# Optimization experiments

Hardware: AMD Instinct MI355X
Metric: run time of the kernel (lower is better)

Reference implementation:

```python
import jax, jax.numpy as jnp
import numpy as np

NUM_CLUSTERS = 56
HEIGHT = 224
WIDTH = 224
BATCH = 32
FEAT_C = 64


def setup_inputs() -> dict:
    key = jax.random.key(0)
    combined_features = jax.random.normal(key, (BATCH, FEAT_C + 1, HEIGHT, WIDTH), dtype=jnp.float32)
    # std parameter init: num_clusters / sqrt(H*W)
    std = jnp.asarray(NUM_CLUSTERS / (HEIGHT * WIDTH) ** 0.5, dtype=jnp.float32)
    return {"combined_features": combined_features, "std": std}


def _sobel(edges):
    # edges: [B,1,H,W], 3x3 sobel with padding=1 (fixed, non-learnable filters)
    kx = jnp.array([[-1., 0., 1.], [-2., 0., 2.], [-1., 0., 1.]], jnp.float32)[None, None]
    ky = jnp.array([[-1., -2., -1.], [0., 0., 0.], [1., 2., 1.]], jnp.float32)[None, None]
    conv = lambda k: jax.lax.conv_general_dilated(edges, k, (1, 1), [(1, 1), (1, 1)])
    return conv(kx), conv(ky)


def reference(combined_features, std):
    B, Cp1, H, W = combined_features.shape
    K = NUM_CLUSTERS
    edges = combined_features[:, -1:]      # [B,1,H,W]
    features = combined_features[:, :-1]   # [B,C,H,W]

    # --- centroid seeding from edge map ---
    Gx, Gy = _sobel(edges)
    grad_mag = jnp.sqrt(Gx ** 2 + Gy ** 2)
    inverted = 1.0 - 0.5 * grad_mag                      # [B,1,H,W]
    # adaptive_avg_pool2d to (K,K); H,W divisible by K -> exact reshape-mean
    pooled = inverted[:, 0].reshape(B, K, H // K, K, W // K).mean(axis=(2, 4))  # [B,K,K]
    flat = pooled.reshape(B, K * K)
    _, idx = jax.lax.top_k(flat, K)                      # [B,K]
    sy = (idx // K).astype(jnp.float32) / K              # [B,K] in [0,1)
    sx = (idx % K).astype(jnp.float32) / K

    # --- spatial gaussian distance: separable over y and x ---
    y = (jnp.arange(H, dtype=jnp.float32) / H)[None, None, :, None]  # [1,1,H,1]
    x = (jnp.arange(W, dtype=jnp.float32) / W)[None, None, None, :]  # [1,1,1,W]
    dy = y - sy[:, :, None, None]                        # [B,K,H,1]
    dx = x - sx[:, :, None, None]                        # [B,K,1,W]
    # gauss2d(a,b,std) = (exp(-(a/std)^2) + exp(-(b/std)^2)) / 2
    spatial = (jnp.exp(-(dy / std) ** 2) + jnp.exp(-(dx / std) ** 2)) * 0.5  # [B,K,H,W]

    # --- feature distance of each pixel to global mean feature (eps=1e-6 as in F.pairwise_distance) ---
    centroid = features.mean(axis=(2, 3))                # [B,C]
    fdist = jnp.sqrt(jnp.sum((features - centroid[:, :, None, None] + 1e-6) ** 2, axis=1))  # [B,H,W]

    combined = spatial + fdist[:, None]                  # [B,K,H,W]
    markers = jax.nn.softmax(combined, axis=1)           # softmax over clusters
    return markers
```

## Files before the change

kernel.cpp:

```cpp
#include <hip/hip_runtime.h>
#include <math.h>

#define NCLUS 56
#define HH 224
#define WW 224
#define BB 32
#define CELLS (NCLUS * NCLUS)
#define HW (HH * WW)

typedef float f32x4 __attribute__((ext_vector_type(4)));

__global__ __launch_bounds__(256) void pool_kernel(const float* __restrict__ cf,
                                                   float* __restrict__ pooled) {
    __shared__ float lds[18][226];
    int b = blockIdx.x / 14;
    int grp = blockIdx.x - b * 14;
    int tid = threadIdx.x;
    const float* e = cf + ((size_t)b * 65 + 64) * HW;

    int y0 = grp * 16 - 1;
    for (int t = tid; t < 18 * 224; t += 256) {
        int r = t / 224;
        int c = t - r * 224;
        int y = y0 + r;
        lds[r][c + 1] = (y >= 0 && y < HH) ? e[y * WW + c] : 0.0f;
    }
    if (tid < 18) { lds[tid][0] = 0.0f; lds[tid][225] = 0.0f; }
    __syncthreads();

    if (tid >= 224) return;
    int lby = tid / 56;
    int bx = tid - lby * 56;
    int r0 = lby * 4;
    int c0 = bx * 4;

    float patch[6][6];
#pragma unroll
    for (int i = 0; i < 6; ++i)
#pragma unroll
        for (int j = 0; j < 6; ++j) patch[i][j] = lds[r0 + i][c0 + j];

    float s = 0.0f;
#pragma unroll
    for (int iy = 0; iy < 4; ++iy) {
#pragma unroll
        for (int ix = 0; ix < 4; ++ix) {
            float gx = (patch[iy][ix + 2] - patch[iy][ix])
                     + 2.0f * (patch[iy + 1][ix + 2] - patch[iy + 1][ix])
                     + (patch[iy + 2][ix + 2] - patch[iy + 2][ix]);
            float gy = (patch[iy + 2][ix] - patch[iy][ix])
                     + 2.0f * (patch[iy + 2][ix + 1] - patch[iy][ix + 1])
                     + (patch[iy + 2][ix + 2] - patch[iy][ix + 2]);
            float gm = sqrtf(gx * gx + gy * gy);
            s += 1.0f - 0.5f * gm;
        }
    }
    pooled[b * CELLS + (grp * 4 + lby) * NCLUS + bx] = s * 0.0625f;
}

__global__ __launch_bounds__(256) void topk_tables_kernel(
        const float* __restrict__ pooled, const float* __restrict__ stdp,
        float* __restrict__ Fx, float* __restrict__ Fy) {
    int b = blockIdx.x;
    int tid = threadIdx.x;
    __shared__ unsigned long long list[CELLS];
    __shared__ float sy_s[NCLUS], sx_s[NCLUS];
    __shared__ unsigned nlist_s;
    if (tid == 0) nlist_s = 0;

    if (tid < 64) {
        unsigned hi[49];
#pragma unroll
        for (int j = 0; j < 49; ++j) {
            int i = j * 64 + tid;
            unsigned u = __float_as_uint(pooled[b * CELLS + i]);
            hi[j] = (u & 0x80000000u) ? ~u : (u | 0x80000000u);
        }
        unsigned prefix = 0;
        unsigned cnt = CELLS;
        for (int bit = 31; bit >= 0; --bit) {
            if (cnt <= 448u) break;
            unsigned cand = prefix | (1u << bit);
            unsigned c = 0;
#pragma unroll
            for (int j = 0; j < 49; ++j) c += (hi[j] >= cand) ? 1u : 0u;
#pragma unroll
            for (int off = 32; off >= 1; off >>= 1)
                c += __shfl_xor(c, off, 64);
            if (c >= (unsigned)NCLUS) { prefix = cand; cnt = c; }
        }
#pragma unroll
        for (int j = 0; j < 49; ++j) {
            if (hi[j] >= prefix) {
                unsigned pos = atomicAdd(&nlist_s, 1u);
                unsigned i = (unsigned)(j * 64 + tid);
                list[pos] = ((unsigned long long)hi[j] << 32) |
                            (unsigned long long)(0xFFFFFFFFu - i);
            }
        }
    }
    __syncthreads();

    int N = (int)nlist_s;
    for (int c = tid; c < N; c += 256) {
        unsigned long long key = list[c];
        int r = 0;
        for (int j = 0; j < N; ++j) r += (list[j] > key) ? 1 : 0;
        if (r < NCLUS) {
            unsigned idx = 0xFFFFFFFFu - (unsigned)(key & 0xFFFFFFFFull);
            sy_s[r] = (float)(idx / NCLUS) / (float)NCLUS;
            sx_s[r] = (float)(idx % NCLUS) / (float)NCLUS;
        }
    }
    __syncthreads();

    float inv_std = 1.0f / stdp[0];
    for (int t = tid; t < NCLUS * WW; t += 256) {
        int k = t / WW;
        int w = t - k * WW;
        float tx = ((float)w / 224.0f - sx_s[k]) * inv_std;
        Fx[(size_t)b * NCLUS * WW + t] = expf(0.5f * expf(-(tx * tx)));
    }
    for (int t = tid; t < HH * NCLUS; t += 256) {
        int h = t / NCLUS;
        int k = t - h * NCLUS;
        float ty = ((float)h / 224.0f - sy_s[k]) * inv_std;
        Fy[(size_t)b * HH * NCLUS + t] = expf(0.5f * expf(-(ty * ty)));
    }
}

__global__ __launch_bounds__(448, 7) void markers_kernel(
        const float* __restrict__ Fx, const float* __restrict__ Fy,
        float* __restrict__ out) {
    __shared__ float fy_s[8 * NCLUS];
    int blk = blockIdx.x;
    int b = blk / 28;
    int h0 = (blk - b * 28) * 8;
    int tid = threadIdx.x;

    fy_s[tid] = Fy[((size_t)b * HH + h0) * NCLUS + tid];
    __syncthreads();

    int row = tid / 56;
    int wq = tid - row * 56;
    const float* fyp = fy_s + row * NCLUS;
    const f32x4* fxp = (const f32x4*)(Fx + (size_t)b * NCLUS * WW) + wq;

    float s0 = 0.f, s1 = 0.f, s2 = 0.f, s3 = 0.f;
#pragma unroll 8
    for (int k = 0; k < NCLUS; ++k) {
        float fy = fyp[k];
        f32x4 fx = fxp[(size_t)k * 56];
        s0 = fmaf(fy, fx.x, s0);
        s1 = fmaf(fy, fx.y, s1);
        s2 = fmaf(fy, fx.z, s2);
        s3 = fmaf(fy, fx.w, s3);
    }
    float r0 = 1.0f / s0, r1 = 1.0f / s1, r2 = 1.0f / s2, r3 = 1.0f / s3;

    float* op = out + (size_t)b * NCLUS * HW + (size_t)(h0 + row) * WW + wq * 4;
#pragma unroll 8
    for (int k = 0; k < NCLUS; ++k) {
        float fy = fyp[k];
        f32x4 fx = fxp[(size_t)k * 56];
        f32x4 o;
        o.x = (fy * fx.x) * r0;
        o.y = (fy * fx.y) * r1;
        o.z = (fy * fx.z) * r2;
        o.w = (fy * fx.w) * r3;
        __builtin_nontemporal_store(o, (f32x4*)op);
        op += HW;
    }
}

extern "C" void kernel_launch(void* const* d_in, const int* in_sizes, int n_in,
                              void* d_out, int out_size, void* d_ws,
                              size_t ws_size, hipStream_t stream) {
    const float* cf = (const float*)d_in[0];
    const float* stdp = (const float*)d_in[1];
    float* out = (float*)d_out;

    char* ws = (char*)d_ws;
    float* pooled = (float*)ws;
    float* Fx = (float*)(ws + 512 * 1024);
    float* Fy = (float*)(ws + 512 * 1024 + 2 * 1024 * 1024);

    pool_kernel<<<BB * 14, 256, 0, stream>>>(cf, pooled);
    topk_tables_kernel<<<BB, 256, 0, stream>>>(pooled, stdp, Fx, Fy);
    markers_kernel<<<BB * 28, 448, 0, stream>>>(Fx, Fy, out);
}
```

Measured before the change: 113.0 us.

## Split markers into reciprocal-sum pass and per-cluster contiguous scale pass

The single markers kernel is replaced by two passes. The first computes the per-pixel softmax denominators with Fx staged in LDS and writes their reciprocals to a workspace buffer. The second writes each cluster plane as one contiguous stream, rereading those reciprocals, with a block-to-XCD mapping that keeps one batch on one XCD so the rereads can hit cache. A transposed Fy table is added and the top-k candidate threshold is lowered; the cost is an extra launch and extra traffic for the intermediate buffer.

```diff
diff --git a/kernel.cpp b/kernel.cpp
--- a/kernel.cpp
+++ b/kernel.cpp
@@ -60,7 +60,8 @@
 
 __global__ __launch_bounds__(256) void topk_tables_kernel(
         const float* __restrict__ pooled, const float* __restrict__ stdp,
-        float* __restrict__ Fx, float* __restrict__ Fy) {
+        float* __restrict__ Fx, float* __restrict__ Fy,
+        float* __restrict__ FyT) {
     int b = blockIdx.x;
     int tid = threadIdx.x;
     __shared__ unsigned long long list[CELLS];
@@ -79,7 +80,7 @@
         unsigned prefix = 0;
         unsigned cnt = CELLS;
         for (int bit = 31; bit >= 0; --bit) {
-            if (cnt <= 448u) break;
+            if (cnt <= 128u) break;
             unsigned cand = prefix | (1u << bit);
             unsigned c = 0;
 #pragma unroll
@@ -127,49 +128,89 @@
         float ty = ((float)h / 224.0f - sy_s[k]) * inv_std;
         Fy[(size_t)b * HH * NCLUS + t] = expf(0.5f * expf(-(ty * ty)));
     }
-}
-
-__global__ __launch_bounds__(448, 7) void markers_kernel(
+    for (int t = tid; t < NCLUS * HH; t += 256) {
+        int k = t / HH;
+        int h = t - k * HH;
+        float ty = ((float)h / 224.0f - sy_s[k]) * inv_std;
+        FyT[(size_t)b * NCLUS * HH + t] = expf(0.5f * expf(-(ty * ty)));
+    }
+}
+
+__global__ __launch_bounds__(448) void sums_kernel(
         const float* __restrict__ Fx, const float* __restrict__ Fy,
-        float* __restrict__ out) {
+        float* __restrict__ Sinv) {
+    __shared__ float fx_lds[NCLUS][WW];
     __shared__ float fy_s[8 * NCLUS];
-    int blk = blockIdx.x;
-    int b = blk / 28;
-    int h0 = (blk - b * 28) * 8;
-    int tid = threadIdx.x;
-
+    int xcd = blockIdx.x & 7;
+    int r = blockIdx.x >> 3;
+    int bq = r / 28;
+    int band = r - bq * 28;
+    int b = bq * 8 + xcd;
+    int h0 = band * 8;
+    int tid = threadIdx.x;
+
+    const f32x4* fxg = (const f32x4*)(Fx + (size_t)b * NCLUS * WW);
+    f32x4* fxl = (f32x4*)&fx_lds[0][0];
+    for (int t = tid; t < NCLUS * WW / 4; t += 448) fxl[t] = fxg[t];
     fy_s[tid] = Fy[((size_t)b * HH + h0) * NCLUS + tid];
     __syncthreads();
 
     int row = tid / 56;
     int wq = tid - row * 56;
     const float* fyp = fy_s + row * NCLUS;
-    const f32x4* fxp = (const f32x4*)(Fx + (size_t)b * NCLUS * WW) + wq;
 
     float s0 = 0.f, s1 = 0.f, s2 = 0.f, s3 = 0.f;
 #pragma unroll 8
     for (int k = 0; k < NCLUS; ++k) {
         float fy = fyp[k];
-        f32x4 fx = fxp[(size_t)k * 56];
+        f32x4 fx = *(const f32x4*)&fx_lds[k][wq * 4];
         s0 = fmaf(fy, fx.x, s0);
         s1 = fmaf(fy, fx.y, s1);
         s2 = fmaf(fy, fx.z, s2);
         s3 = fmaf(fy, fx.w, s3);
     }
-    float r0 = 1.0f / s0, r1 = 1.0f / s1, r2 = 1.0f / s2, r3 = 1.0f / s3;
-
-    float* op = out + (size_t)b * NCLUS * HW + (size_t)(h0 + row) * WW + wq * 4;
-#pragma unroll 8
-    for (int k = 0; k < NCLUS; ++k) {
-        float fy = fyp[k];
-        f32x4 fx = fxp[(size_t)k * 56];
+    f32x4 rv;
+    rv.x = 1.0f / s0;
+    rv.y = 1.0f / s1;
+    rv.z = 1.0f / s2;
+    rv.w = 1.0f / s3;
+    *(f32x4*)(Sinv + (size_t)b * HW + (size_t)(h0 + row) * WW + wq * 4) = rv;
+}
+
+__global__ __launch_bounds__(256) void scale_kernel(
+        const float* __restrict__ Fx, const float* __restrict__ FyT,
+        const float* __restrict__ Sinv, float* __restrict__ out) {
+    __shared__ float fx_l[WW];
+    __shared__ float fy_l[HH];
+    int xcd = blockIdx.x & 7;
+    int r = blockIdx.x >> 3;
+    int bq = r / 56;
+    int k = r - bq * 56;
+    int b = bq * 8 + xcd;
+    int tid = threadIdx.x;
+
+    if (tid < 224) {
+        fx_l[tid] = Fx[((size_t)b * NCLUS + k) * WW + tid];
+        fy_l[tid] = FyT[((size_t)b * NCLUS + k) * HH + tid];
+    }
+    __syncthreads();
+
+    const f32x4* sp = (const f32x4*)(Sinv + (size_t)b * HW);
+    f32x4* op = (f32x4*)(out + ((size_t)b * NCLUS + k) * HW);
+#pragma unroll 7
+    for (int i = 0; i < 49; ++i) {
+        int e = i * 256 + tid;
+        int h = e / 56;
+        int w4 = e - h * 56;
+        f32x4 sv = sp[e];
+        float fy = fy_l[h];
+        f32x4 fx = *(const f32x4*)&fx_l[w4 * 4];
         f32x4 o;
-        o.x = (fy * fx.x) * r0;
-        o.y = (fy * fx.y) * r1;
-        o.z = (fy * fx.z) * r2;
-        o.w = (fy * fx.w) * r3;
-        __builtin_nontemporal_store(o, (f32x4*)op);
-        op += HW;
+        o.x = (fy * fx.x) * sv.x;
+        o.y = (fy * fx.y) * sv.y;
+        o.z = (fy * fx.z) * sv.z;
+        o.w = (fy * fx.w) * sv.w;
+        __builtin_nontemporal_store(o, op + e);
     }
 }
 
@@ -182,10 +223,13 @@
 
     char* ws = (char*)d_ws;
     float* pooled = (float*)ws;
-    float* Fx = (float*)(ws + 512 * 1024);
-    float* Fy = (float*)(ws + 512 * 1024 + 2 * 1024 * 1024);
+    float* Sinv   = (float*)ws;
+    float* Fx  = (float*)(ws + 7 * 1024 * 1024);
+    float* Fy  = (float*)(ws + 9 * 1024 * 1024);
+    float* FyT = (float*)(ws + 11 * 1024 * 1024);
 
     pool_kernel<<<BB * 14, 256, 0, stream>>>(cf, pooled);
-    topk_tables_kernel<<<BB, 256, 0, stream>>>(pooled, stdp, Fx, Fy);
-    markers_kernel<<<BB * 28, 448, 0, stream>>>(Fx, Fy, out);
-}
+    topk_tables_kernel<<<BB, 256, 0, stream>>>(pooled, stdp, Fx, Fy, FyT);
+    sums_kernel<<<BB * 28, 448, 0, stream>>>(Fx, Fy, Sinv);
+    scale_kernel<<<BB * NCLUS, 256, 0, stream>>>(Fx, FyT, Sinv, out);
+}
```

Result: slower. 121.9 us (+7.9%).

## Split markers into sums and scale kernels with LDS-staged Fx tables

Applied to the files above, without the earlier changes.

Separates computing the per-pixel softmax normalizer into its own kernel that writes inverse sums to workspace. A second kernel writes outputs with each block handling half of the clusters, doubling the block count, and stages Fx rows in LDS. The top-k candidate threshold is also lowered to shrink the rank-sort list. This adds an extra launch and a round trip through a workspace buffer in exchange for more write parallelism.

```diff
diff --git a/kernel.cpp b/kernel.cpp
--- a/kernel.cpp
+++ b/kernel.cpp
@@ -7,6 +7,7 @@
 #define BB 32
 #define CELLS (NCLUS * NCLUS)
 #define HW (HH * WW)
+#define KSPL 28
 
 typedef float f32x4 __attribute__((ext_vector_type(4)));
 
@@ -79,7 +80,7 @@
         unsigned prefix = 0;
         unsigned cnt = CELLS;
         for (int bit = 31; bit >= 0; --bit) {
-            if (cnt <= 448u) break;
+            if (cnt <= 128u) break;
             unsigned cand = prefix | (1u << bit);
             unsigned c = 0;
 #pragma unroll
@@ -129,45 +130,89 @@
     }
 }
 
-__global__ __launch_bounds__(448, 7) void markers_kernel(
+__global__ __launch_bounds__(448) void sums_kernel(
         const float* __restrict__ Fx, const float* __restrict__ Fy,
-        float* __restrict__ out) {
+        float* __restrict__ Sinv) {
+    __shared__ float fx_lds[NCLUS][WW];
     __shared__ float fy_s[8 * NCLUS];
     int blk = blockIdx.x;
     int b = blk / 28;
     int h0 = (blk - b * 28) * 8;
     int tid = threadIdx.x;
 
+    const f32x4* fxg = (const f32x4*)(Fx + (size_t)b * NCLUS * WW);
+    f32x4* fxl = (f32x4*)&fx_lds[0][0];
+#pragma unroll
+    for (int t = 0; t < 7; ++t) fxl[t * 448 + tid] = fxg[t * 448 + tid];
     fy_s[tid] = Fy[((size_t)b * HH + h0) * NCLUS + tid];
     __syncthreads();
 
     int row = tid / 56;
     int wq = tid - row * 56;
     const float* fyp = fy_s + row * NCLUS;
-    const f32x4* fxp = (const f32x4*)(Fx + (size_t)b * NCLUS * WW) + wq;
 
     float s0 = 0.f, s1 = 0.f, s2 = 0.f, s3 = 0.f;
 #pragma unroll 8
     for (int k = 0; k < NCLUS; ++k) {
         float fy = fyp[k];
-        f32x4 fx = fxp[(size_t)k * 56];
+        f32x4 fx = *(const f32x4*)&fx_lds[k][wq * 4];
         s0 = fmaf(fy, fx.x, s0);
         s1 = fmaf(fy, fx.y, s1);
         s2 = fmaf(fy, fx.z, s2);
         s3 = fmaf(fy, fx.w, s3);
     }
-    float r0 = 1.0f / s0, r1 = 1.0f / s1, r2 = 1.0f / s2, r3 = 1.0f / s3;
-
-    float* op = out + (size_t)b * NCLUS * HW + (size_t)(h0 + row) * WW + wq * 4;
-#pragma unroll 8
-    for (int k = 0; k < NCLUS; ++k) {
-        float fy = fyp[k];
-        f32x4 fx = fxp[(size_t)k * 56];
+    f32x4 rv;
+    rv.x = 1.0f / s0;
+    rv.y = 1.0f / s1;
+    rv.z = 1.0f / s2;
+    rv.w = 1.0f / s3;
+    *(f32x4*)(Sinv + (size_t)b * HW + (size_t)(h0 + row) * WW + wq * 4) = rv;
+}
+
+__global__ __launch_bounds__(448) void scale_kernel(
+        const float* __restrict__ Fx, const float* __restrict__ Fy,
+        const float* __restrict__ Sinv, float* __restrict__ out) {
+    __shared__ float fx_lds[KSPL][WW];
+    __shared__ float fy_s[8 * KSPL];
+    int blk = blockIdx.x;
+    int b = blk / 56;
+    int r = blk - b * 56;
+    int band = r >> 1;
+    int half = r & 1;
+    int h0 = band * 8;
+    int k0 = half * KSPL;
+    int tid = threadIdx.x;
+
+    int row = tid / 56;
+    int wq = tid - row * 56;
+
+    f32x4 sv = *(const f32x4*)(Sinv + (size_t)b * HW +
+                               (size_t)(h0 + row) * WW + wq * 4);
+
+    const f32x4* fxg = (const f32x4*)(Fx + ((size_t)b * NCLUS + k0) * WW);
+    f32x4* fxl = (f32x4*)&fx_lds[0][0];
+#pragma unroll
+    for (int t = 0; t < 3; ++t) fxl[t * 448 + tid] = fxg[t * 448 + tid];
+    if (tid < 224) fxl[3 * 448 + tid] = fxg[3 * 448 + tid];
+    if (tid < 8 * KSPL) {
+        int rr = tid / KSPL;
+        int kk = tid - rr * KSPL;
+        fy_s[tid] = Fy[((size_t)b * HH + h0 + rr) * NCLUS + k0 + kk];
+    }
+    __syncthreads();
+
+    const float* fyp = fy_s + row * KSPL;
+    float* op = out + ((size_t)b * NCLUS + k0) * HW +
+                (size_t)(h0 + row) * WW + wq * 4;
+#pragma unroll 7
+    for (int kk = 0; kk < KSPL; ++kk) {
+        float fy = fyp[kk];
+        f32x4 fx = *(const f32x4*)&fx_lds[kk][wq * 4];
         f32x4 o;
-        o.x = (fy * fx.x) * r0;
-        o.y = (fy * fx.y) * r1;
-        o.z = (fy * fx.z) * r2;
-        o.w = (fy * fx.w) * r3;
+        o.x = (fy * fx.x) * sv.x;
+        o.y = (fy * fx.y) * sv.y;
+        o.z = (fy * fx.z) * sv.z;
+        o.w = (fy * fx.w) * sv.w;
         __builtin_nontemporal_store(o, (f32x4*)op);
         op += HW;
     }
@@ -182,10 +227,12 @@
 
     char* ws = (char*)d_ws;
     float* pooled = (float*)ws;
-    float* Fx = (float*)(ws + 512 * 1024);
-    float* Fy = (float*)(ws + 512 * 1024 + 2 * 1024 * 1024);
+    float* Sinv = (float*)(ws + 1 * 1024 * 1024);
+    float* Fx = (float*)(ws + 8 * 1024 * 1024);
+    float* Fy = (float*)(ws + 10 * 1024 * 1024);
 
     pool_kernel<<<BB * 14, 256, 0, stream>>>(cf, pooled);
     topk_tables_kernel<<<BB, 256, 0, stream>>>(pooled, stdp, Fx, Fy);
-    markers_kernel<<<BB * 28, 448, 0, stream>>>(Fx, Fy, out);
-}
+    sums_kernel<<<BB * 28, 448, 0, stream>>>(Fx, Fy, Sinv);
+    scale_kernel<<<BB * NCLUS, 448, 0, stream>>>(Fx, Fy, Sinv, out);
+}
```

Measured after the change: 118.2 us. +4.6%, slower.
